# Performance work log

Hardware: AMD Instinct MI355X
Metric: run time of the kernel (lower is better)

## Reference

```python
import jax, jax.numpy as jnp
import numpy as np

N_NODES = 100000
N_EDGES = 400000
IN_F, HID, OUT_F = 128, 1024, 64


def gcn_conv(x, src, dst, ew, W, b, n):
    # PyG GCNConv: add self-loops (weight 1), symmetric normalization,
    # out[dst] += norm * (x @ W)[src], then bias.
    loop = jnp.arange(n)
    s = jnp.concatenate([src, loop])
    d = jnp.concatenate([dst, loop])
    w = jnp.concatenate([ew, jnp.ones((n,), dtype=ew.dtype)])
    deg = jax.ops.segment_sum(w, d, num_segments=n)
    dinv = jnp.where(deg > 0, jax.lax.rsqrt(deg), 0.0)
    norm = dinv[s] * w * dinv[d]                      # [E+N]
    h = x @ W                                         # [N, out]
    out = jax.ops.segment_sum(h[s] * norm[:, None], d, num_segments=n)
    return out + b


def setup_inputs() -> dict:
    key = jax.random.key(0)
    k = jax.random.split(key, 8)
    x = jax.random.normal(k[0], (N_NODES, IN_F), dtype=jnp.float32)
    edge_index = jax.random.randint(k[1], (2, N_EDGES), 0, N_NODES, dtype=jnp.int64)
    edge_weight = jax.random.uniform(k[2], (N_EDGES,), dtype=jnp.float32)
    # Glorot-ish init for params
    W1 = jax.random.normal(k[3], (IN_F, HID), dtype=jnp.float32) * (1.0 / np.sqrt(IN_F))
    b1 = jnp.zeros((HID,), dtype=jnp.float32)
    W2 = jax.random.normal(k[4], (HID, OUT_F), dtype=jnp.float32) * (1.0 / np.sqrt(HID))
    b2 = jnp.zeros((OUT_F,), dtype=jnp.float32)
    return {"x": x, "edge_index": edge_index, "edge_weight": edge_weight,
            "W1": W1, "b1": b1, "W2": W2, "b2": b2}


def reference(x, edge_index, edge_weight, W1, b1, W2, b2):
    src, dst = edge_index[0], edge_index[1]
    h = gcn_conv(x, src, dst, edge_weight, W1, b1, N_NODES)
    h = jax.nn.relu(h)
    # F.dropout with training=False is identity (eval mode)
    out = gcn_conv(h, src, dst, edge_weight, W2, b2, N_NODES)
    return out
```

## Files before the change

kernel.cpp:

```cpp
#include <hip/hip_runtime.h>
#include <hip/hip_bf16.h>

#define N_NODES 100000
#define N_EDGES 400000
#define IN_F    128
#define HID     1024
#define OUT_F   64
#define BUCKET_CAP 24

typedef __attribute__((ext_vector_type(8))) short short8;
typedef __attribute__((ext_vector_type(4))) float floatx4;

__device__ inline unsigned short f2bf(float f) {
    unsigned int u = __float_as_uint(f);
    unsigned int r = u + 0x7FFF + ((u >> 16) & 1);
    return (unsigned short)(r >> 16);
}

__device__ inline unsigned int cvtpk(float a, float b) {
    union { __hip_bfloat162 h; unsigned int u; } v;
    v.h = __float22bfloat162_rn(float2{a, b});
    return v.u;
}

__device__ inline float bf2f(unsigned int lo16) {
    return __uint_as_float(lo16 << 16);
}

__device__ __forceinline__ void gload_lds16(const void* g, void* l) {
    __builtin_amdgcn_global_load_lds(
        (const __attribute__((address_space(1))) void*)g,
        (__attribute__((address_space(3))) void*)l, 16, 0, 0);
}


__global__ void init_kernel(float* __restrict__ deg, int* __restrict__ cnt, int n) {
    int i = blockIdx.x * blockDim.x + threadIdx.x;
    if (i < n) { deg[i] = 1.0f; cnt[i] = 0; }
}

__global__ void deg_accum_kernel(const int* __restrict__ dst, const float* __restrict__ w,
                                 float* __restrict__ deg, int E) {
    int e = blockIdx.x * blockDim.x + threadIdx.x;
    if (e < E) atomicAdd(&deg[dst[e]], w[e]);
}

__global__ void rsqrt_inplace_kernel(float* __restrict__ deg, int n) {
    int i = blockIdx.x * blockDim.x + threadIdx.x;
    if (i < n) deg[i] = rsqrtf(deg[i]);
}

__global__ void fill_pairs_kernel(const int* __restrict__ src, const int* __restrict__ dst,
                                  const float* __restrict__ w, const float* __restrict__ dinv,
                                  int* __restrict__ cnt, int2* __restrict__ pairs, int E) {
    int e = blockIdx.x * blockDim.x + threadIdx.x;
    if (e < E) {
        int s = src[e];
        int d = dst[e];
        float nv = dinv[s] * w[e] * dinv[d];
        int slot = atomicAdd(&cnt[d], 1);
        if (slot < BUCKET_CAP)
            pairs[(long)d * BUCKET_CAP + slot] = make_int2(s, __float_as_int(nv));
    }
}


__global__ void convert_xb_kernel(const float* __restrict__ in, unsigned short* __restrict__ out, long n8) {
    long i = (long)blockIdx.x * blockDim.x + threadIdx.x;
    if (i < n8) {
        float4 a = ((const float4*)in)[i * 2];
        float4 b = ((const float4*)in)[i * 2 + 1];
        ((uint4*)out)[i] = make_uint4(cvtpk(a.x, a.y), cvtpk(a.z, a.w),
                                      cvtpk(b.x, b.y), cvtpk(b.z, b.w));
    }
}


__global__ __launch_bounds__(256) void gather128_kernel(
    const int2* __restrict__ pairs, const int* __restrict__ cnt,
    const float* __restrict__ dinv, const unsigned short* __restrict__ xb,
    unsigned short* __restrict__ xab)
{
    int node = blockIdx.x * 8 + (threadIdx.x >> 5);
    int l = threadIdx.x & 31;
    float di = dinv[node];
    float s = di * di;
    uint2 uv = ((const uint2*)(xb + (long)node * IN_F))[l];
    float4 acc;
    acc.x = bf2f(uv.x & 0xffffu) * s;
    acc.y = bf2f(uv.x >> 16) * s;
    acc.z = bf2f(uv.y & 0xffffu) * s;
    acc.w = bf2f(uv.y >> 16) * s;
    int c = cnt[node]; c = c < BUCKET_CAP ? c : BUCKET_CAP;
    const int2* p = pairs + (long)node * BUCKET_CAP;
    int j = 0;
    for (; j + 4 <= c; j += 4) {
        int4 q01 = *(const int4*)(p + j);
        int4 q23 = *(const int4*)(p + j + 2);
        uint2 u0 = ((const uint2*)(xb + (long)q01.x * IN_F))[l];
        uint2 u1 = ((const uint2*)(xb + (long)q01.z * IN_F))[l];
        uint2 u2 = ((const uint2*)(xb + (long)q23.x * IN_F))[l];
        uint2 u3 = ((const uint2*)(xb + (long)q23.z * IN_F))[l];
        float n0 = __int_as_float(q01.y), n1 = __int_as_float(q01.w);
        float n2 = __int_as_float(q23.y), n3 = __int_as_float(q23.w);
        acc.x += n0 * bf2f(u0.x & 0xffffu) + n1 * bf2f(u1.x & 0xffffu)
               + n2 * bf2f(u2.x & 0xffffu) + n3 * bf2f(u3.x & 0xffffu);
        acc.y += n0 * bf2f(u0.x >> 16) + n1 * bf2f(u1.x >> 16)
               + n2 * bf2f(u2.x >> 16) + n3 * bf2f(u3.x >> 16);
        acc.z += n0 * bf2f(u0.y & 0xffffu) + n1 * bf2f(u1.y & 0xffffu)
               + n2 * bf2f(u2.y & 0xffffu) + n3 * bf2f(u3.y & 0xffffu);
        acc.w += n0 * bf2f(u0.y >> 16) + n1 * bf2f(u1.y >> 16)
               + n2 * bf2f(u2.y >> 16) + n3 * bf2f(u3.y >> 16);
    }
    for (; j < c; j++) {
        int2 pp = p[j];
        float nv = __int_as_float(pp.y);
        uint2 u = ((const uint2*)(xb + (long)pp.x * IN_F))[l];
        acc.x += nv * bf2f(u.x & 0xffffu);
        acc.y += nv * bf2f(u.x >> 16);
        acc.z += nv * bf2f(u.y & 0xffffu);
        acc.w += nv * bf2f(u.y >> 16);
    }
    uint2 pk;
    pk.x = cvtpk(acc.x, acc.y);
    pk.y = cvtpk(acc.z, acc.w);
    ((uint2*)(xab + (long)node * IN_F))[l] = pk;
}

__global__ __launch_bounds__(256) void gather64_kernel(
    const int2* __restrict__ pairs, const int* __restrict__ cnt,
    const float* __restrict__ dinv, const unsigned short* __restrict__ tb,
    const float* __restrict__ bias, float* __restrict__ out)
{
    int node = blockIdx.x * 8 + (threadIdx.x >> 5);
    int l = threadIdx.x & 31;
    float di = dinv[node];
    float s = di * di;
    unsigned int tv = ((const unsigned int*)(tb + (long)node * OUT_F))[l];
    float2 bb = ((const float2*)bias)[l];
    float2 acc;
    acc.x = bf2f(tv & 0xffffu) * s + bb.x;
    acc.y = bf2f(tv >> 16) * s + bb.y;
    int c = cnt[node]; c = c < BUCKET_CAP ? c : BUCKET_CAP;
    const int2* p = pairs + (long)node * BUCKET_CAP;
    int j = 0;
    for (; j + 4 <= c; j += 4) {
        int4 q01 = *(const int4*)(p + j);
        int4 q23 = *(const int4*)(p + j + 2);
        unsigned int u0 = ((const unsigned int*)(tb + (long)q01.x * OUT_F))[l];
        unsigned int u1 = ((const unsigned int*)(tb + (long)q01.z * OUT_F))[l];
        unsigned int u2 = ((const unsigned int*)(tb + (long)q23.x * OUT_F))[l];
        unsigned int u3 = ((const unsigned int*)(tb + (long)q23.z * OUT_F))[l];
        float n0 = __int_as_float(q01.y), n1 = __int_as_float(q01.w);
        float n2 = __int_as_float(q23.y), n3 = __int_as_float(q23.w);
        acc.x += n0 * bf2f(u0 & 0xffffu) + n1 * bf2f(u1 & 0xffffu)
               + n2 * bf2f(u2 & 0xffffu) + n3 * bf2f(u3 & 0xffffu);
        acc.y += n0 * bf2f(u0 >> 16) + n1 * bf2f(u1 >> 16)
               + n2 * bf2f(u2 >> 16) + n3 * bf2f(u3 >> 16);
    }
    for (; j < c; j++) {
        int2 pp = p[j];
        float nv = __int_as_float(pp.y);
        unsigned int u = ((const unsigned int*)(tb + (long)pp.x * OUT_F))[l];
        acc.x += nv * bf2f(u & 0xffffu);
        acc.y += nv * bf2f(u >> 16);
    }
    ((float2*)(out + (long)node * OUT_F))[l] = acc;
}


__global__ void convert_wstream_kernel(const float* __restrict__ W1, const float* __restrict__ W2,
                                       unsigned short* __restrict__ S) {
    int r = blockIdx.x * blockDim.x + threadIdx.x;
    int c = blockIdx.y;
    int f = r >> 9;
    int l = (r >> 3) & 63;
    int j = r & 7;
    float v;
    if (f < 16) {
        int nt = f >> 2, kt = f & 3;
        int hid = c * 64 + nt * 16 + (l & 15);
        int k   = kt * 32 + (l >> 4) * 8 + j;
        v = W1[(long)k * HID + hid];
    } else {
        int f2 = f - 16;
        int kb = f2 >> 2, nt2 = f2 & 3;
        int kh = c * 64 + kb * 32 + (j >> 2) * 16 + (l >> 4) * 4 + (j & 3);
        int oc = nt2 * 16 + (l & 15);
        v = W2[(long)kh * OUT_F + oc];
    }
    S[(long)c * 12288 + r] = f2bf(v);
}


__global__ __launch_bounds__(512, 4) void fused_mlp_mfma_kernel(
    const unsigned short* __restrict__ Xb, const unsigned short* __restrict__ Wstream,
    const float* __restrict__ b1, unsigned short* __restrict__ Tb, int M)
{
    __shared__ unsigned short Wbuf[2][12288];

    const int tid = threadIdx.x;
    const int w   = tid >> 6;
    const int l   = tid & 63;
    const int lr  = l & 15;
    const int lq  = l >> 4;
    const long row0 = (long)blockIdx.x * 256 + w * 32;

    short8 bx[2][4];
    #pragma unroll
    for (int rt = 0; rt < 2; rt++) {
        long row = row0 + rt * 16 + lr;
        if (row < M) {
            const unsigned short* p = Xb + row * IN_F + lq * 8;
            #pragma unroll
            for (int kt = 0; kt < 4; kt++)
                bx[rt][kt] = *(const short8*)(p + kt * 32);
        } else {
            #pragma unroll
            for (int kt = 0; kt < 4; kt++)
                #pragma unroll
                for (int j = 0; j < 8; j++) bx[rt][kt][j] = 0;
        }
    }

    {
        const unsigned short* g = Wstream + (long)(w * 3) * 512 + l * 8;
        unsigned short* d = &Wbuf[0][(w * 3) * 512];
        #pragma unroll
        for (int s = 0; s < 3; s++)
            gload_lds16(g + s * 512, d + s * 512);
    }
    __syncthreads();

    floatx4 tacc[2][4];
    #pragma unroll
    for (int rt = 0; rt < 2; rt++)
        #pragma unroll
        for (int nt = 0; nt < 4; nt++)
            tacc[rt][nt] = (floatx4)0.0f;

    for (int c = 0; c < 16; c++) {
        const unsigned short* Wb = &Wbuf[c & 1][0];

        if (c < 15) {
            const unsigned short* g = Wstream + (long)(c + 1) * 12288 + (long)(w * 3) * 512 + l * 8;
            unsigned short* d = &Wbuf[(c + 1) & 1][(w * 3) * 512];
            #pragma unroll
            for (int s = 0; s < 3; s++)
                gload_lds16(g + s * 512, d + s * 512);
        }

        #pragma unroll
        for (int h = 0; h < 2; h++) {
            floatx4 hacc[2][2];
            #pragma unroll
            for (int rt = 0; rt < 2; rt++)
                #pragma unroll
                for (int n = 0; n < 2; n++)
                    hacc[rt][n] = (floatx4)0.0f;

            #pragma unroll
            for (int n = 0; n < 2; n++) {
                const int nt = h * 2 + n;
                short8 w1f[4];
                #pragma unroll
                for (int kt = 0; kt < 4; kt++)
                    w1f[kt] = *(const short8*)(Wb + (nt * 4 + kt) * 512 + l * 8);
                #pragma unroll
                for (int kt = 0; kt < 4; kt++) {
                    hacc[0][n] = __builtin_amdgcn_mfma_f32_16x16x32_bf16(w1f[kt], bx[0][kt], hacc[0][n], 0, 0, 0);
                    hacc[1][n] = __builtin_amdgcn_mfma_f32_16x16x32_bf16(w1f[kt], bx[1][kt], hacc[1][n], 0, 0, 0);
                }
            }

            floatx4 bb0 = *(const floatx4*)(b1 + c * 64 + (h * 2 + 0) * 16 + lq * 4);
            floatx4 bb1 = *(const floatx4*)(b1 + c * 64 + (h * 2 + 1) * 16 + lq * 4);
            short8 hf[2];
            #pragma unroll
            for (int rt = 0; rt < 2; rt++) {
                #pragma unroll
                for (int r = 0; r < 4; r++) {
                    hf[rt][r]     = (short)f2bf(fmaxf(hacc[rt][0][r] + bb0[r], 0.0f));
                    hf[rt][r + 4] = (short)f2bf(fmaxf(hacc[rt][1][r] + bb1[r], 0.0f));
                }
            }

            #pragma unroll
            for (int nt2 = 0; nt2 < 4; nt2++) {
                short8 w2f = *(const short8*)(Wb + (16 + h * 4 + nt2) * 512 + l * 8);
                tacc[0][nt2] = __builtin_amdgcn_mfma_f32_16x16x32_bf16(w2f, hf[0], tacc[0][nt2], 0, 0, 0);
                tacc[1][nt2] = __builtin_amdgcn_mfma_f32_16x16x32_bf16(w2f, hf[1], tacc[1][nt2], 0, 0, 0);
            }
        }

        if (c < 15) __syncthreads();
    }

    #pragma unroll
    for (int rt = 0; rt < 2; rt++) {
        long row = row0 + rt * 16 + lr;
        if (row < M) {
            #pragma unroll
            for (int nt = 0; nt < 4; nt++) {
                unsigned int q0 = (unsigned int)f2bf(tacc[rt][nt][0]) | ((unsigned int)f2bf(tacc[rt][nt][1]) << 16);
                unsigned int q1 = (unsigned int)f2bf(tacc[rt][nt][2]) | ((unsigned int)f2bf(tacc[rt][nt][3]) << 16);
                *(uint2*)(Tb + row * OUT_F + nt * 16 + lq * 4) = make_uint2(q0, q1);
            }
        }
    }
}


extern "C" void kernel_launch(void* const* d_in, const int* in_sizes, int n_in,
                              void* d_out, int out_size, void* d_ws, size_t ws_size,
                              hipStream_t stream) {
    const float* x   = (const float*)d_in[0];
    const int*   src = (const int*)d_in[1];
    const int*   dst = ((const int*)d_in[1]) + N_EDGES;
    const float* ew  = (const float*)d_in[2];
    const float* W1  = (const float*)d_in[3];
    const float* b1  = (const float*)d_in[4];
    const float* W2  = (const float*)d_in[5];
    const float* b2  = (const float*)d_in[6];
    float* out = (float*)d_out;

    float* ws     = (float*)d_ws;
    float* dinv   = ws;
    int*   cnt    = (int*)(ws + 100096);
    int2*  pairs  = (int2*)(ws + 200192);
    unsigned short* xb  = (unsigned short*)(ws + 5000192);
    unsigned short* xab = (unsigned short*)(ws + 11400192);
    unsigned short* tb  = (unsigned short*)(ws + 17800192);
    unsigned short* wstream = (unsigned short*)(ws + 21000192);

    const int B = 256;

    init_kernel<<<(N_NODES + B - 1) / B, B, 0, stream>>>(dinv, cnt, N_NODES);
    deg_accum_kernel<<<(N_EDGES + B - 1) / B, B, 0, stream>>>(dst, ew, dinv, N_EDGES);
    convert_xb_kernel<<<(int)(((long)N_NODES * IN_F / 8 + B - 1) / B), B, 0, stream>>>(
        x, xb, (long)N_NODES * IN_F / 8);
    convert_wstream_kernel<<<dim3(48, 16), B, 0, stream>>>(W1, W2, wstream);
    rsqrt_inplace_kernel<<<(N_NODES + B - 1) / B, B, 0, stream>>>(dinv, N_NODES);
    fill_pairs_kernel<<<(N_EDGES + B - 1) / B, B, 0, stream>>>(src, dst, ew, dinv, cnt, pairs, N_EDGES);

    gather128_kernel<<<N_NODES / 8, 256, 0, stream>>>(pairs, cnt, dinv, xb, xab);

    fused_mlp_mfma_kernel<<<(N_NODES + 255) / 256, 512, 0, stream>>>(
        xab, wstream, b1, tb, N_NODES);

    gather64_kernel<<<N_NODES / 8, 256, 0, stream>>>(pairs, cnt, dinv, tb, b2, out);
}
```

Before: 170.5 us.

## Read MLP weights directly from global memory and fold rsqrt into consumers

The fused MLP kernel no longer double-buffers the weight stream through LDS with async global-to-LDS loads and per-chunk barriers. Each wave now reads its weight fragments straight from global memory, relying on L1/L2 caching, and blocks shrink to 256 threads covering 128 rows. The separate rsqrt kernel is also removed: consumers compute rsqrtf(deg) inline, saving one launch and one pass over the nodes. The trade-off is extra rsqrt work per edge and more global/cache traffic for weights in exchange for removing LDS staging and synchronization.

```diff
diff --git a/kernel.cpp b/kernel.cpp
--- a/kernel.cpp
+++ b/kernel.cpp
@@ -27,12 +27,6 @@
     return __uint_as_float(lo16 << 16);
 }
 
-__device__ __forceinline__ void gload_lds16(const void* g, void* l) {
-    __builtin_amdgcn_global_load_lds(
-        (const __attribute__((address_space(1))) void*)g,
-        (__attribute__((address_space(3))) void*)l, 16, 0, 0);
-}
-
 
 __global__ void init_kernel(float* __restrict__ deg, int* __restrict__ cnt, int n) {
     int i = blockIdx.x * blockDim.x + threadIdx.x;
@@ -45,19 +39,14 @@
     if (e < E) atomicAdd(&deg[dst[e]], w[e]);
 }
 
-__global__ void rsqrt_inplace_kernel(float* __restrict__ deg, int n) {
-    int i = blockIdx.x * blockDim.x + threadIdx.x;
-    if (i < n) deg[i] = rsqrtf(deg[i]);
-}
-
 __global__ void fill_pairs_kernel(const int* __restrict__ src, const int* __restrict__ dst,
-                                  const float* __restrict__ w, const float* __restrict__ dinv,
+                                  const float* __restrict__ w, const float* __restrict__ deg,
                                   int* __restrict__ cnt, int2* __restrict__ pairs, int E) {
     int e = blockIdx.x * blockDim.x + threadIdx.x;
     if (e < E) {
         int s = src[e];
         int d = dst[e];
-        float nv = dinv[s] * w[e] * dinv[d];
+        float nv = rsqrtf(deg[s]) * w[e] * rsqrtf(deg[d]);
         int slot = atomicAdd(&cnt[d], 1);
         if (slot < BUCKET_CAP)
             pairs[(long)d * BUCKET_CAP + slot] = make_int2(s, __float_as_int(nv));
@@ -78,12 +67,12 @@
 
 __global__ __launch_bounds__(256) void gather128_kernel(
     const int2* __restrict__ pairs, const int* __restrict__ cnt,
-    const float* __restrict__ dinv, const unsigned short* __restrict__ xb,
+    const float* __restrict__ deg, const unsigned short* __restrict__ xb,
     unsigned short* __restrict__ xab)
 {
     int node = blockIdx.x * 8 + (threadIdx.x >> 5);
     int l = threadIdx.x & 31;
-    float di = dinv[node];
+    float di = rsqrtf(deg[node]);
     float s = di * di;
     uint2 uv = ((const uint2*)(xb + (long)node * IN_F))[l];
     float4 acc;
@@ -129,12 +118,12 @@
 
 __global__ __launch_bounds__(256) void gather64_kernel(
     const int2* __restrict__ pairs, const int* __restrict__ cnt,
-    const float* __restrict__ dinv, const unsigned short* __restrict__ tb,
+    const float* __restrict__ deg, const unsigned short* __restrict__ tb,
     const float* __restrict__ bias, float* __restrict__ out)
 {
     int node = blockIdx.x * 8 + (threadIdx.x >> 5);
     int l = threadIdx.x & 31;
-    float di = dinv[node];
+    float di = rsqrtf(deg[node]);
     float s = di * di;
     unsigned int tv = ((const unsigned int*)(tb + (long)node * OUT_F))[l];
     float2 bb = ((const float2*)bias)[l];
@@ -193,18 +182,16 @@
 }
 
 
-__global__ __launch_bounds__(512, 4) void fused_mlp_mfma_kernel(
+__global__ __launch_bounds__(256) void fused_mlp_mfma_kernel(
     const unsigned short* __restrict__ Xb, const unsigned short* __restrict__ Wstream,
     const float* __restrict__ b1, unsigned short* __restrict__ Tb, int M)
 {
-    __shared__ unsigned short Wbuf[2][12288];
-
     const int tid = threadIdx.x;
     const int w   = tid >> 6;
     const int l   = tid & 63;
     const int lr  = l & 15;
     const int lq  = l >> 4;
-    const long row0 = (long)blockIdx.x * 256 + w * 32;
+    const long row0 = (long)blockIdx.x * 128 + w * 32;
 
     short8 bx[2][4];
     #pragma unroll
@@ -223,15 +210,6 @@
         }
     }
 
-    {
-        const unsigned short* g = Wstream + (long)(w * 3) * 512 + l * 8;
-        unsigned short* d = &Wbuf[0][(w * 3) * 512];
-        #pragma unroll
-        for (int s = 0; s < 3; s++)
-            gload_lds16(g + s * 512, d + s * 512);
-    }
-    __syncthreads();
-
     floatx4 tacc[2][4];
     #pragma unroll
     for (int rt = 0; rt < 2; rt++)
@@ -239,16 +217,10 @@
         for (int nt = 0; nt < 4; nt++)
             tacc[rt][nt] = (floatx4)0.0f;
 
+    const unsigned short* wlane = Wstream + l * 8;
+
     for (int c = 0; c < 16; c++) {
-        const unsigned short* Wb = &Wbuf[c & 1][0];
-
-        if (c < 15) {
-            const unsigned short* g = Wstream + (long)(c + 1) * 12288 + (long)(w * 3) * 512 + l * 8;
-            unsigned short* d = &Wbuf[(c + 1) & 1][(w * 3) * 512];
-            #pragma unroll
-            for (int s = 0; s < 3; s++)
-                gload_lds16(g + s * 512, d + s * 512);
-        }
+        const unsigned short* Wc = wlane + (long)c * 12288;
 
         #pragma unroll
         for (int h = 0; h < 2; h++) {
@@ -265,7 +237,7 @@
                 short8 w1f[4];
                 #pragma unroll
                 for (int kt = 0; kt < 4; kt++)
-                    w1f[kt] = *(const short8*)(Wb + (nt * 4 + kt) * 512 + l * 8);
+                    w1f[kt] = *(const short8*)(Wc + (nt * 4 + kt) * 512);
                 #pragma unroll
                 for (int kt = 0; kt < 4; kt++) {
                     hacc[0][n] = __builtin_amdgcn_mfma_f32_16x16x32_bf16(w1f[kt], bx[0][kt], hacc[0][n], 0, 0, 0);
@@ -287,13 +259,11 @@
 
             #pragma unroll
             for (int nt2 = 0; nt2 < 4; nt2++) {
-                short8 w2f = *(const short8*)(Wb + (16 + h * 4 + nt2) * 512 + l * 8);
+                short8 w2f = *(const short8*)(Wc + (16 + h * 4 + nt2) * 512);
                 tacc[0][nt2] = __builtin_amdgcn_mfma_f32_16x16x32_bf16(w2f, hf[0], tacc[0][nt2], 0, 0, 0);
                 tacc[1][nt2] = __builtin_amdgcn_mfma_f32_16x16x32_bf16(w2f, hf[1], tacc[1][nt2], 0, 0, 0);
             }
         }
-
-        if (c < 15) __syncthreads();
     }
 
     #pragma unroll
@@ -325,7 +295,7 @@
     float* out = (float*)d_out;
 
     float* ws     = (float*)d_ws;
-    float* dinv   = ws;
+    float* deg    = ws;
     int*   cnt    = (int*)(ws + 100096);
     int2*  pairs  = (int2*)(ws + 200192);
     unsigned short* xb  = (unsigned short*)(ws + 5000192);
@@ -335,18 +305,17 @@
 
     const int B = 256;
 
-    init_kernel<<<(N_NODES + B - 1) / B, B, 0, stream>>>(dinv, cnt, N_NODES);
-    deg_accum_kernel<<<(N_EDGES + B - 1) / B, B, 0, stream>>>(dst, ew, dinv, N_EDGES);
+    init_kernel<<<(N_NODES + B - 1) / B, B, 0, stream>>>(deg, cnt, N_NODES);
+    deg_accum_kernel<<<(N_EDGES + B - 1) / B, B, 0, stream>>>(dst, ew, deg, N_EDGES);
     convert_xb_kernel<<<(int)(((long)N_NODES * IN_F / 8 + B - 1) / B), B, 0, stream>>>(
         x, xb, (long)N_NODES * IN_F / 8);
     convert_wstream_kernel<<<dim3(48, 16), B, 0, stream>>>(W1, W2, wstream);
-    rsqrt_inplace_kernel<<<(N_NODES + B - 1) / B, B, 0, stream>>>(dinv, N_NODES);
-    fill_pairs_kernel<<<(N_EDGES + B - 1) / B, B, 0, stream>>>(src, dst, ew, dinv, cnt, pairs, N_EDGES);
-
-    gather128_kernel<<<N_NODES / 8, 256, 0, stream>>>(pairs, cnt, dinv, xb, xab);
-
-    fused_mlp_mfma_kernel<<<(N_NODES + 255) / 256, 512, 0, stream>>>(
+    fill_pairs_kernel<<<(N_EDGES + B - 1) / B, B, 0, stream>>>(src, dst, ew, deg, cnt, pairs, N_EDGES);
+
+    gather128_kernel<<<N_NODES / 8, 256, 0, stream>>>(pairs, cnt, deg, xb, xab);
+
+    fused_mlp_mfma_kernel<<<(N_NODES + 127) / 128, 256, 0, stream>>>(
         xab, wstream, b1, tb, N_NODES);
 
-    gather64_kernel<<<N_NODES / 8, 256, 0, stream>>>(pairs, cnt, dinv, tb, b2, out);
-}
+    gather64_kernel<<<N_NODES / 8, 256, 0, stream>>>(pairs, cnt, deg, tb, b2, out);
+}
```

Measured after the change: 224.6 us. 31.7% more time.
